# Optimization experiments

Hardware: AMD Instinct MI355X
Metric: run time of the kernel (lower is better)

The kernel has to match this reference:

```python
import jax, jax.numpy as jnp
import numpy as np

N_NODES = 100000


def setup_inputs() -> dict:
    key = jax.random.key(0)
    k1, k2, k3, k4, k5 = jax.random.split(key, 5)
    d_in, d_out, n_edges = 128, 128, 640000
    x = jax.random.normal(k1, (N_NODES, d_in), dtype=jnp.float32)
    edge_index = jax.random.randint(k2, (2, n_edges), 0, N_NODES, dtype=jnp.int64)
    # uniform(size, W) in the source is U(-1/sqrt(in), 1/sqrt(in)); scaled normal is fine as data
    s = 1.0 / np.sqrt(d_in)
    Wc = jax.random.normal(k3, (d_in, d_out), dtype=jnp.float32) * s
    Wn = jax.random.normal(k4, (d_in, d_out), dtype=jnp.float32) * s
    b = jax.random.normal(k5, (d_out,), dtype=jnp.float32) * s
    return {"x": x, "edge_index": edge_index, "Wc": Wc, "Wn": Wn, "b": b}


def reference(x, edge_index, Wc, Wn, b):
    row, col = edge_index[0], edge_index[1]
    alpha = x @ Wc                      # [N, out]
    beta = x @ Wn                       # [N, out]
    # Vectorized scatter-mean replacing the original per-node Python loop:
    # gamma[n] = mean(beta[col[row == n]])
    num = jax.ops.segment_sum(beta[col], row, num_segments=N_NODES)   # [N, out]
    cnt = jax.ops.segment_sum(jnp.ones_like(row, dtype=beta.dtype), row, num_segments=N_NODES)
    gamma = num / jnp.maximum(cnt, 1.0)[:, None]  # NOTE: unused below, exactly as in the original forward
    del gamma
    # The original returns alpha + beta + bias (gamma is dead code in the source).
    return alpha + beta + b
```

## Files before the change

### kernel.cpp

```cpp
#include <hip/hip_runtime.h>


#define NROWS 100000

typedef __attribute__((ext_vector_type(8))) __bf16 bf16x8;
typedef __attribute__((ext_vector_type(8))) unsigned short u16x8;
typedef __attribute__((ext_vector_type(4))) float f32x4;

__device__ __forceinline__ bf16x8 pack8(const float4 lo, const float4 hi) {
    bf16x8 r;
    r[0] = (__bf16)lo.x; r[1] = (__bf16)lo.y; r[2] = (__bf16)lo.z; r[3] = (__bf16)lo.w;
    r[4] = (__bf16)hi.x; r[5] = (__bf16)hi.y; r[6] = (__bf16)hi.z; r[7] = (__bf16)hi.w;
    return r;
}

__global__ void prep_wt(const float* __restrict__ Wc, const float* __restrict__ Wn,
                        unsigned short* __restrict__ wt) {
    int i = blockIdx.x * 256 + threadIdx.x;
    int n = i >> 7, k = i & 127;
    __bf16 v = (__bf16)(Wc[k * 128 + n] + Wn[k * 128 + n]);
    wt[i] = __builtin_bit_cast(unsigned short, v);
}

__global__ __launch_bounds__(256) void gemm_bias(
    const float* __restrict__ x, const unsigned short* __restrict__ wt,
    const float* __restrict__ bias_g, float* __restrict__ out) {

    __shared__ __align__(16) unsigned short sWt[128 * 136];

    const int tid = threadIdx.x;
    #pragma unroll
    for (int it = 0; it < 8; ++it) {
        int idx8 = it * 256 + tid;
        int n = idx8 >> 4;
        int k = (idx8 & 15) << 3;
        *(u16x8*)&sWt[n * 136 + k] = *(const u16x8*)(wt + (idx8 << 3));
    }
    __syncthreads();

    const int wave = tid >> 6;
    const int lane = tid & 63;
    const int quad = lane >> 4;
    const int l16  = lane & 15;

    const long rowbase = (long)blockIdx.x * 128 + wave * 32;
    if (rowbase >= NROWS) return;

    f32x4 acc[2][8] = {};

    const float* xr0 = x + (rowbase + l16) * 128;
    const float* xr1 = xr0 + 16 * 128;

    #pragma unroll
    for (int kc = 0; kc < 4; ++kc) {
        const int ko = kc * 32 + quad * 8;
        float4 a0lo = *(const float4*)(xr0 + ko);
        float4 a0hi = *(const float4*)(xr0 + ko + 4);
        float4 a1lo = *(const float4*)(xr1 + ko);
        float4 a1hi = *(const float4*)(xr1 + ko + 4);
        bf16x8 a0 = pack8(a0lo, a0hi);
        bf16x8 a1 = pack8(a1lo, a1hi);
        #pragma unroll
        for (int ct = 0; ct < 8; ++ct) {
            bf16x8 wf = *(const bf16x8*)&sWt[(ct * 16 + l16) * 136 + ko];
            acc[0][ct] = __builtin_amdgcn_mfma_f32_16x16x32_bf16(wf, a0, acc[0][ct], 0, 0, 0);
            acc[1][ct] = __builtin_amdgcn_mfma_f32_16x16x32_bf16(wf, a1, acc[1][ct], 0, 0, 0);
        }
    }

    float4 bv[8];
    #pragma unroll
    for (int ct = 0; ct < 8; ++ct)
        bv[ct] = *(const float4*)(bias_g + ct * 16 + quad * 4);

    #pragma unroll
    for (int mt = 0; mt < 2; ++mt) {
        float* orow = out + (rowbase + mt * 16 + l16) * 128;
        #pragma unroll
        for (int ct = 0; ct < 8; ++ct) {
            float4 st4;
            st4.x = acc[mt][ct][0] + bv[ct].x;
            st4.y = acc[mt][ct][1] + bv[ct].y;
            st4.z = acc[mt][ct][2] + bv[ct].z;
            st4.w = acc[mt][ct][3] + bv[ct].w;
            *(float4*)(orow + ct * 16 + quad * 4) = st4;
        }
    }
}

extern "C" void kernel_launch(void* const* d_in, const int* in_sizes, int n_in,
                              void* d_out, int out_size, void* d_ws, size_t ws_size,
                              hipStream_t stream) {
    const float* x  = (const float*)d_in[0];
    const float* Wc = (const float*)d_in[2];
    const float* Wn = (const float*)d_in[3];
    const float* b  = (const float*)d_in[4];
    unsigned short* wt = (unsigned short*)d_ws;
    float* out = (float*)d_out;

    prep_wt<<<64, 256, 0, stream>>>(Wc, Wn, wt);
    const int nblocks = (NROWS + 127) / 128;
    gemm_bias<<<nblocks, 256, 0, stream>>>(x, wt, b, out);
}
```

Measured before the change: 114.8 us.

## Prefetch weights and x rows before the LDS barrier and use nontemporal output stores

Weight tiles are loaded into registers and all x rows for the wave are loaded and packed to bf16 before the weights are written to shared memory and the block barrier. The global load latency for x now overlaps the weight staging instead of following the barrier. Inactive waves clamp their row base so they still take part in the barrier. Output stores become nontemporal to avoid polluting cache, at the cost of higher register pressure from holding staged data.

```diff
diff --git a/kernel.cpp b/kernel.cpp
--- a/kernel.cpp
+++ b/kernel.cpp
@@ -28,43 +28,57 @@
 
     __shared__ __align__(16) unsigned short sWt[128 * 136];
 
-    const int tid = threadIdx.x;
-    #pragma unroll
-    for (int it = 0; it < 8; ++it) {
-        int idx8 = it * 256 + tid;
-        int n = idx8 >> 4;
-        int k = (idx8 & 15) << 3;
-        *(u16x8*)&sWt[n * 136 + k] = *(const u16x8*)(wt + (idx8 << 3));
-    }
-    __syncthreads();
-
+    const int tid  = threadIdx.x;
     const int wave = tid >> 6;
     const int lane = tid & 63;
     const int quad = lane >> 4;
     const int l16  = lane & 15;
 
+    u16x8 stg[8];
+    #pragma unroll
+    for (int it = 0; it < 8; ++it) {
+        const int idx8 = it * 256 + tid;
+        stg[it] = *(const u16x8*)(wt + (idx8 << 3));
+    }
+
     const long rowbase = (long)blockIdx.x * 128 + wave * 32;
-    if (rowbase >= NROWS) return;
-
-    f32x4 acc[2][8] = {};
-
-    const float* xr0 = x + (rowbase + l16) * 128;
+    const bool active  = rowbase < NROWS;
+    const long rb      = active ? rowbase : (NROWS - 32);
+    const float* xr0 = x + (rb + l16) * 128;
     const float* xr1 = xr0 + 16 * 128;
 
+    bf16x8 a0[4], a1[4];
     #pragma unroll
     for (int kc = 0; kc < 4; ++kc) {
         const int ko = kc * 32 + quad * 8;
-        float4 a0lo = *(const float4*)(xr0 + ko);
-        float4 a0hi = *(const float4*)(xr0 + ko + 4);
-        float4 a1lo = *(const float4*)(xr1 + ko);
-        float4 a1hi = *(const float4*)(xr1 + ko + 4);
-        bf16x8 a0 = pack8(a0lo, a0hi);
-        bf16x8 a1 = pack8(a1lo, a1hi);
+        float4 lo0 = *(const float4*)(xr0 + ko);
+        float4 hi0 = *(const float4*)(xr0 + ko + 4);
+        float4 lo1 = *(const float4*)(xr1 + ko);
+        float4 hi1 = *(const float4*)(xr1 + ko + 4);
+        a0[kc] = pack8(lo0, hi0);
+        a1[kc] = pack8(lo1, hi1);
+    }
+
+    #pragma unroll
+    for (int it = 0; it < 8; ++it) {
+        const int idx8 = it * 256 + tid;
+        const int n = idx8 >> 4;
+        const int k = (idx8 & 15) << 3;
+        *(u16x8*)&sWt[n * 136 + k] = stg[it];
+    }
+    __syncthreads();
+
+    if (!active) return;
+
+    f32x4 acc[2][8] = {};
+    #pragma unroll
+    for (int kc = 0; kc < 4; ++kc) {
+        const int ko = kc * 32 + quad * 8;
         #pragma unroll
         for (int ct = 0; ct < 8; ++ct) {
             bf16x8 wf = *(const bf16x8*)&sWt[(ct * 16 + l16) * 136 + ko];
-            acc[0][ct] = __builtin_amdgcn_mfma_f32_16x16x32_bf16(wf, a0, acc[0][ct], 0, 0, 0);
-            acc[1][ct] = __builtin_amdgcn_mfma_f32_16x16x32_bf16(wf, a1, acc[1][ct], 0, 0, 0);
+            acc[0][ct] = __builtin_amdgcn_mfma_f32_16x16x32_bf16(wf, a0[kc], acc[0][ct], 0, 0, 0);
+            acc[1][ct] = __builtin_amdgcn_mfma_f32_16x16x32_bf16(wf, a1[kc], acc[1][ct], 0, 0, 0);
         }
     }
 
@@ -78,12 +92,12 @@
         float* orow = out + (rowbase + mt * 16 + l16) * 128;
         #pragma unroll
         for (int ct = 0; ct < 8; ++ct) {
-            float4 st4;
-            st4.x = acc[mt][ct][0] + bv[ct].x;
-            st4.y = acc[mt][ct][1] + bv[ct].y;
-            st4.z = acc[mt][ct][2] + bv[ct].z;
-            st4.w = acc[mt][ct][3] + bv[ct].w;
-            *(float4*)(orow + ct * 16 + quad * 4) = st4;
+            f32x4 st4 = acc[mt][ct];
+            st4[0] += bv[ct].x;
+            st4[1] += bv[ct].y;
+            st4[2] += bv[ct].z;
+            st4[3] += bv[ct].w;
+            __builtin_nontemporal_store(st4, (f32x4*)(orow + ct * 16 + quad * 4));
         }
     }
 }
```

Measured after the change: 118.4 us. 3.1% more time.
